# Performance work log

Hardware: AMD Instinct MI355X
Metric: run time of the kernel (lower is better)

Reference implementation:

```python
import jax, jax.numpy as jnp
import numpy as np

POI, EMB, UNITS, QDIM, B = 5000, 256, 512, 256, 64


def setup_inputs() -> dict:
    key = jax.random.key(0)
    ks = jax.random.split(key, 16)
    s = 0.05
    return {
        "x": jax.random.randint(ks[0], (B,), 0, POI),
        "query": jax.random.normal(ks[1], (B, QDIM), jnp.float32),
        "poi_embedding": jax.random.normal(ks[2], (POI, EMB), jnp.float32),
        "A_hat": jax.random.normal(ks[3], (B, B), jnp.float32),
        "dec_hidden": jax.random.normal(ks[4], (B, UNITS), jnp.float32),
        "cat_dec_hidden": jax.random.normal(ks[5], (1, B, UNITS), jnp.float32),
        # GRUCell params (keras order z, r, h; reset_after=True -> bias [2, 3*units])
        "gru_kernel": jax.random.normal(ks[6], (EMB + QDIM, 3 * UNITS), jnp.float32) * s,
        "gru_rec_kernel": jax.random.normal(ks[7], (UNITS, 3 * UNITS), jnp.float32) * s,
        "gru_bias": jax.random.normal(ks[8], (2, 3 * UNITS), jnp.float32) * s,
        # Bahdanau attention params
        "W1_w": jax.random.normal(ks[9], (EMB, UNITS), jnp.float32) * s,
        "W1_b": jnp.zeros((UNITS,), jnp.float32),
        "W2_w": jax.random.normal(ks[10], (UNITS, UNITS), jnp.float32) * s,
        "W2_b": jnp.zeros((UNITS,), jnp.float32),
        "V_w": jax.random.normal(ks[11], (UNITS, 1), jnp.float32) * s,
        "V_b": jnp.zeros((1,), jnp.float32),
        # output dense: concat(context EMB, output_ UNITS, cat_hidden UNITS) -> POI
        "fc_w": jax.random.normal(ks[12], (EMB + 2 * UNITS, POI), jnp.float32) * s,
        "fc_b": jnp.zeros((POI,), jnp.float32),
    }


def _gru_cell(x, h, kernel, rec_kernel, bias):
    # keras GRUCell, reset_after=True, gate order (z, r, h)
    xm = x @ kernel + bias[0]        # [B, 3U]
    hm = h @ rec_kernel + bias[1]    # [B, 3U]
    xz, xr, xh = jnp.split(xm, 3, axis=-1)
    hz, hr, hh = jnp.split(hm, 3, axis=-1)
    z = jax.nn.sigmoid(xz + hz)
    r = jax.nn.sigmoid(xr + hr)
    h_cand = jnp.tanh(xh + r * hh)
    h_new = z * h + (1.0 - z) * h_cand
    return h_new, h_new


def reference(x, query, poi_embedding, A_hat, dec_hidden, cat_dec_hidden,
              gru_kernel, gru_rec_kernel, gru_bias,
              W1_w, W1_b, W2_w, W2_b, V_w, V_b, fc_w, fc_b):
    emb = poi_embedding
    x1 = jnp.concatenate([emb[x], query], axis=1)          # [B, EMB+QDIM]
    output_, state = _gru_cell(x1, dec_hidden, gru_kernel, gru_rec_kernel, gru_bias)
    # Bahdanau attention: values are the full embedding table [POI, EMB]
    v_proj = emb @ W1_w + W1_b                              # [POI, U]
    q_proj = output_ @ W2_w + W2_b                          # [B, U]
    score = jnp.tanh(v_proj[None, :, :] + q_proj[:, None, :]) @ V_w + V_b  # [B, POI, 1]
    attn = jax.nn.softmax(score, axis=1)                    # [B, POI, 1]
    context = jnp.sum(attn * emb[None, :, :], axis=1)       # [B, EMB]
    out_cat = jnp.concatenate([context, output_, cat_dec_hidden[0]], axis=1)
    logits = out_cat @ fc_w + fc_b                          # [B, POI]
    return (logits, state, output_)
```

## Files before the change

kernel.cpp:

```cpp
#include <hip/hip_runtime.h>
#include <hip/hip_bf16.h>

typedef __bf16 bf16;
typedef __bf16 bf16x8 __attribute__((ext_vector_type(8)));
typedef float f32x4 __attribute__((ext_vector_type(4)));
typedef float f32x2 __attribute__((ext_vector_type(2)));

#define BB 64
#define EMB 256
#define UNITS 512
#define POI 5000
#define KCAT 1280
#define SCLD 5024
#define L2E 1.4426950408889634f

__device__ __forceinline__ float rcp_(float x){ return __builtin_amdgcn_rcpf(x); }
__device__ __forceinline__ float exp2_(float x){ return __builtin_amdgcn_exp2f(x); }

__device__ __forceinline__ bf16x8 cvt8(f32x4 a0, f32x4 a1){
  bf16x8 o;
#pragma unroll
  for(int j=0;j<4;j++){ o[j]=(bf16)a0[j]; o[4+j]=(bf16)a1[j]; }
  return o;
}

__device__ __forceinline__ f32x4 mm16r(const float* __restrict__ ap, const float* __restrict__ B,
                                       int ldb, int K, int nc, int lane){
  int q = lane >> 4;
  f32x4 acc = {0.f,0.f,0.f,0.f};
  ap += q*8;
  const float* bp = B + (size_t)(q*8)*ldb + nc;
#pragma unroll 2
  for(int k0 = 0; k0 < K; k0 += 32){
    bf16x8 a = cvt8(*(const f32x4*)ap, *(const f32x4*)(ap+4));
    bf16x8 b;
#pragma unroll
    for(int j=0;j<8;j++) b[j] = (bf16)bp[(size_t)j*ldb];
    acc = __builtin_amdgcn_mfma_f32_16x16x32_bf16(a, b, acc, 0, 0, 0);
    ap += 32; bp += (size_t)32*ldb;
  }
  return acc;
}
__device__ __forceinline__ f32x4 mm16f(const float* __restrict__ A, const float* __restrict__ B,
                                       int lda, int ldb, int K, int mr, int nc, int lane){
  return mm16r(A + (size_t)mr*lda, B, ldb, K, nc, lane);
}

__device__ __forceinline__ void t64(const float* __restrict__ src, int srcLd, int nRv,
    int r0, int c0, int cW, bf16* __restrict__ dstT, int dstLd,
    int lane, int w){
  int r = r0 + lane;
  bool rv = r < nRv;
  int cw4 = cW >> 2;
  int cb = c0 + w*cw4;
  for(int c8=0;c8<cw4;c8+=8){
    int c = cb + c8;
    f32x4 v0={0.f,0.f,0.f,0.f}, v1={0.f,0.f,0.f,0.f};
    if(rv){ v0 = *(const f32x4*)(src + (size_t)r*srcLd + c);
            v1 = *(const f32x4*)(src + (size_t)r*srcLd + c + 4); }
#pragma unroll
    for(int j=0;j<4;j++){
      dstT[(size_t)(c+j)*dstLd + r]   = (bf16)v0[j];
      dstT[(size_t)(c+4+j)*dstLd + r] = (bf16)v1[j];
    }
  }
}

__global__ __launch_bounds__(256) void k_prep0(
    const float* __restrict__ emb, const float* __restrict__ W1, const float* __restrict__ W2,
    const float* __restrict__ fcb, const float* __restrict__ catd,
    float* __restrict__ out, float* __restrict__ outc,
    bf16* __restrict__ embB, bf16* __restrict__ W1Tb, bf16* __restrict__ W2Tb,
    float* __restrict__ sumb, float* __restrict__ sc){
  int bx = blockIdx.x, t = threadIdx.x, lane = t & 63, w = t >> 6;
  if(bx < 80){
    int r0 = bx*64;
    for(int ch = t; ch < 2048; ch += 256){
      int r = r0 + (ch >> 5), cc = (ch & 31)*8;
      if(r < POI){
        f32x4 v0 = *(const f32x4*)(emb + (size_t)r*EMB + cc);
        f32x4 v1 = *(const f32x4*)(emb + (size_t)r*EMB + cc + 4);
        *(bf16x8*)(embB + (size_t)r*EMB + cc) = cvt8(v0, v1);
      }
    }
  } else if(bx < 88){
    int i = bx - 80;
    t64(W1, UNITS, EMB, (i>>1)*64, (i&1)*256, 256, W1Tb, EMB, lane, w);
  } else if(bx < 104){
    int i = bx - 88;
    t64(W2, UNITS, UNITS, (i>>1)*64, (i&1)*256, 256, W2Tb, UNITS, lane, w);
  } else if(bx < 168){
    int b = bx - 104;
    for(int n=t; n<POI; n+=256) out[(size_t)b*POI + n] = fcb[n];
  } else if(bx < 176){
    int base = (bx - 168)*8;
    for(int i=t; i<8*768; i+=256){
      int bb = base + i/768, c = i - (i/768)*768;
      if(c < 256) outc[(size_t)bb*KCAT + c] = 0.f;
      else        outc[(size_t)bb*KCAT + 512 + c] = catd[(size_t)bb*512 + (c-256)];
    }
  } else {
    if(t < BB) sumb[t] = 0.f;
    for(int i=t; i<BB*24; i+=256){
      int b = i/24, j = i - (i/24)*24;
      sc[(size_t)b*SCLD + POI + j] = 0.f;
    }
  }
}

__global__ __launch_bounds__(256) void k_gru(const int* __restrict__ x, const float* __restrict__ query,
    const bf16* __restrict__ embB, const float* __restrict__ h0,
    const float* __restrict__ gruK, const float* __restrict__ gruR,
    float* __restrict__ xmP, float* __restrict__ hmP){
  int lane = threadIdx.x & 63, w = threadIdx.x >> 6;
  int col = blockIdx.x*16 + (lane & 15);
  int y = blockIdx.y, z = blockIdx.z;
  int mr = w*16 + (lane & 15);
  int q = lane >> 4;
  const float* bp = (y ? gruR : gruK) + (size_t)(z*256 + q*8)*1536 + col;
  float* C = (y ? hmP : xmP) + (size_t)z*BB*1536;
  f32x4 acc = {0.f,0.f,0.f,0.f};
  if(y == 0 && z == 0){
    const bf16* ap = embB + (size_t)x[mr]*EMB + q*8;
#pragma unroll 2
    for(int k0=0;k0<256;k0+=32){
      bf16x8 a = *(const bf16x8*)ap;
      bf16x8 b;
#pragma unroll
      for(int j=0;j<8;j++) b[j] = (bf16)bp[(size_t)j*1536];
      acc = __builtin_amdgcn_mfma_f32_16x16x32_bf16(a, b, acc, 0,0,0);
      ap += 32; bp += (size_t)32*1536;
    }
  } else {
    const float* apf = y ? (h0 + (size_t)mr*512 + z*256 + q*8)
                         : (query + (size_t)mr*256 + q*8);
#pragma unroll 2
    for(int k0=0;k0<256;k0+=32){
      bf16x8 a = cvt8(*(const f32x4*)apf, *(const f32x4*)(apf+4));
      bf16x8 b;
#pragma unroll
      for(int j=0;j<8;j++) b[j] = (bf16)bp[(size_t)j*1536];
      acc = __builtin_amdgcn_mfma_f32_16x16x32_bf16(a, b, acc, 0,0,0);
      apf += 32; bp += (size_t)32*1536;
    }
  }
  int rb = w*16 + (lane >> 4)*4;
#pragma unroll
  for(int r=0;r<4;r++) C[(size_t)(rb+r)*1536 + col] = acc[r];
}

__global__ __launch_bounds__(256) void k_gates(const float* __restrict__ xmP, const float* __restrict__ hmP,
                        const float* __restrict__ bias, const float* __restrict__ h0,
                        float* __restrict__ hn, float* __restrict__ outc, float* __restrict__ dout){
  int b = blockIdx.x, u = blockIdx.y*256 + threadIdx.x;
  const float* x0 = xmP + b*1536; const float* x1s = xmP + (size_t)BB*1536 + b*1536;
  const float* h0s = hmP + b*1536; const float* h1s = hmP + (size_t)BB*1536 + b*1536;
  float xz = x0[u]      + x1s[u]      + bias[u];
  float xg = x0[512+u]  + x1s[512+u]  + bias[512+u];
  float xh = x0[1024+u] + x1s[1024+u] + bias[1024+u];
  float hz = h0s[u]      + h1s[u]      + bias[1536+u];
  float hg = h0s[512+u]  + h1s[512+u]  + bias[2048+u];
  float hh = h0s[1024+u] + h1s[1024+u] + bias[2560+u];
  float z = rcp_(1.f + exp2_(-L2E*(xz+hz)));
  float r = rcp_(1.f + exp2_(-L2E*(xg+hg)));
  float ca = xh + r*hh;
  ca = fminf(fmaxf(ca, -15.f), 15.f);
  float e = exp2_(2.f*L2E*ca);
  float hc = (e - 1.f)*rcp_(e + 1.f);
  float h = h0[(size_t)b*512+u];
  float v = z*h + (1.f - z)*hc;
  hn[(size_t)b*512+u] = v;
  outc[(size_t)b*KCAT + 256 + u] = v;
  dout[(size_t)POI*BB + (size_t)b*512 + u] = v;
  dout[(size_t)POI*BB + (size_t)BB*512 + (size_t)b*512 + u] = v;
}

__global__ __launch_bounds__(256) void k_qproj(const float* __restrict__ hn, const bf16* __restrict__ W2Tb,
                        const float* __restrict__ W2b, float* __restrict__ Eq){
  __shared__ float accs[16][17];
  int t = threadIdx.x, lane = t & 63, w = t >> 6;
  int c16 = blockIdx.x & 31, r16 = blockIdx.x >> 5;
  for(int i=t;i<16*17;i+=256) ((float*)accs)[i] = 0.f;
  __syncthreads();
  int q = lane >> 4;
  int mr  = r16*16 + (lane & 15);
  int col = c16*16 + (lane & 15);
  const float* ap = hn + (size_t)mr*UNITS + w*128 + q*8;
  const bf16*  bp = W2Tb + (size_t)col*UNITS + w*128 + q*8;
  f32x4 acc = {0.f,0.f,0.f,0.f};
#pragma unroll
  for(int k0=0;k0<128;k0+=32){
    bf16x8 a = cvt8(*(const f32x4*)ap, *(const f32x4*)(ap+4));
    bf16x8 b = *(const bf16x8*)bp;
    acc = __builtin_amdgcn_mfma_f32_16x16x32_bf16(a,b,acc,0,0,0);
    ap += 32; bp += 32;
  }
#pragma unroll
  for(int r=0;r<4;r++) atomicAdd(&accs[q*4+r][lane & 15], acc[r]);
  __syncthreads();
  int r = t >> 4, c = t & 15;
  int colg = c16*16 + c;
  float v = (accs[r][c] + W2b[colg])*(2.f*L2E);
  Eq[(size_t)(r16*16+r)*UNITS + colg] = exp2_(fminf(fmaxf(v,-40.f),40.f));
}

__global__ __launch_bounds__(512) void k_vscore(
    const bf16* __restrict__ embB, const bf16* __restrict__ W1Tb,
    const float* __restrict__ W1b, const float* __restrict__ Eq,
    const float* __restrict__ Vw, float* __restrict__ sc, float* __restrict__ sumb){
  __shared__ float evsT[512][20];
  __shared__ float vws[512];
  int t = threadIdx.x, lane = t & 63, w = t >> 6;
  int p0 = blockIdx.x*16;
  int q = lane >> 4;
  int mr = p0 + (lane & 15); if(mr > POI-1) mr = POI-1;
  bf16x8 afr[8];
  {
    const bf16* ap = embB + (size_t)mr*EMB + q*8;
#pragma unroll
    for(int k=0;k<8;k++){ afr[k] = *(const bf16x8*)ap; ap += 32; }
  }
#pragma unroll
  for(int i=0;i<4;i++){
    int colL = (w + 8*i)*16 + (lane & 15);
    const bf16* bp = W1Tb + (size_t)colL*EMB + q*8;
    f32x4 acc = {0.f,0.f,0.f,0.f};
#pragma unroll
    for(int k=0;k<8;k++){
      acc = __builtin_amdgcn_mfma_f32_16x16x32_bf16(afr[k], *(const bf16x8*)bp, acc, 0,0,0);
      bp += 32;
    }
    float bn = W1b[colL];
    f32x4 ev;
#pragma unroll
    for(int r=0;r<4;r++){
      float v = (acc[r] + bn)*(2.f*L2E);
      ev[r] = exp2_(fminf(fmaxf(v,-40.f),40.f));
    }
    *(f32x4*)&evsT[colL][q*4] = ev;
  }
  vws[t] = Vw[t];
  __syncthreads();
  int pg = t & 7, b = t >> 3;
  const float* qrow = Eq + (size_t)b*UNITS;
  f32x2 s = {0.f, 0.f};
#pragma unroll 4
  for(int u4=0; u4<128; ++u4){
    f32x4 q4 = *(const f32x4*)&qrow[u4*4];
    f32x4 wv = *(const f32x4*)&vws[u4*4];
#pragma unroll
    for(int j=0;j<4;j++){
      f32x2 ev = *(const f32x2*)&evsT[u4*4+j][2*pg];
      s[0] += wv[j]*rcp_(ev[0]*q4[j] + 1.f);
      s[1] += wv[j]*rcp_(ev[1]*q4[j] + 1.f);
    }
  }
  int pA = p0 + 2*pg;
  float e0 = (pA   < POI) ? exp2_(-2.f*L2E*s[0]) : 0.f;
  float e1 = (pA+1 < POI) ? exp2_(-2.f*L2E*s[1]) : 0.f;
  float* srow = sc + (size_t)b*SCLD + pA;
  if(pA+1 < POI){ f32x2 e2 = {e0, e1}; *(f32x2*)srow = e2; }
  else if(pA < POI) srow[0] = e0;
  float ps = e0 + e1;
  ps += __shfl_xor(ps, 1);
  ps += __shfl_xor(ps, 2);
  ps += __shfl_xor(ps, 4);
  if(pg == 0) atomicAdd(&sumb[b], ps);
}

__global__ __launch_bounds__(256) void k_ctx(const float* __restrict__ wb, const float* __restrict__ emb,
                                             const float* __restrict__ sumb, float* __restrict__ outc){
  int lane = threadIdx.x & 63, w = threadIdx.x >> 6;
  int n = blockIdx.x*16 + (lane & 15);
  int ky = blockIdx.y;
  int kbeg = ky*64;
  int mr = w*16 + (lane & 15);
  int q = lane >> 4;
  const float* ap = wb + (size_t)mr*SCLD + kbeg + q*8;
  f32x4 acc = {0.f,0.f,0.f,0.f};
  if(ky < 78){
    const float* bp = emb + (size_t)(kbeg + q*8)*EMB + n;
#pragma unroll 2
    for(int k0=0;k0<64;k0+=32){
      bf16x8 a = cvt8(*(const f32x4*)ap, *(const f32x4*)(ap+4));
      bf16x8 b;
#pragma unroll
      for(int j=0;j<8;j++) b[j] = (bf16)bp[(size_t)j*EMB];
      acc = __builtin_amdgcn_mfma_f32_16x16x32_bf16(a,b,acc,0,0,0);
      ap += 32; bp += (size_t)32*EMB;
    }
  } else {
    bf16x8 a = cvt8(*(const f32x4*)ap, *(const f32x4*)(ap+4));
    bf16x8 b;
#pragma unroll
    for(int j=0;j<8;j++){
      int k = kbeg + q*8 + j; int kc = k < POI ? k : POI-1;
      b[j] = (bf16)emb[(size_t)kc*EMB + n];
    }
    acc = __builtin_amdgcn_mfma_f32_16x16x32_bf16(a,b,acc,0,0,0);
  }
  int rb = w*16 + (lane >> 4)*4;
#pragma unroll
  for(int r=0;r<4;r++) atomicAdd(&outc[(size_t)(rb+r)*KCAT + n], acc[r]*rcp_(sumb[rb+r]));
}

__global__ __launch_bounds__(256) void k_logits(const float* __restrict__ A, const float* __restrict__ Bw,
                        float* __restrict__ out){
  int lane = threadIdx.x & 63, w = threadIdx.x >> 6;
  int n = blockIdx.x*16 + (lane & 15);
  int nc = n < POI ? n : POI-1;
  int ky = blockIdx.y, kbeg = ky*160;
  f32x4 acc = mm16f(A + kbeg, Bw + (size_t)kbeg*POI, KCAT, POI, 160,
                    w*16 + (lane & 15), nc, lane);
  int rb = w*16 + (lane >> 4)*4;
  if(n < POI){
#pragma unroll
    for(int r=0;r<4;r++) atomicAdd(&out[(size_t)(rb+r)*POI + n], acc[r]);
  }
}

extern "C" void kernel_launch(void* const* d_in, const int* in_sizes, int n_in,
                              void* d_out, int out_size, void* d_ws, size_t ws_size,
                              hipStream_t stream){
  const int*   x     = (const int*)d_in[0];
  const float* query = (const float*)d_in[1];
  const float* emb   = (const float*)d_in[2];
  const float* h0    = (const float*)d_in[4];
  const float* catd  = (const float*)d_in[5];
  const float* gruK  = (const float*)d_in[6];
  const float* gruR  = (const float*)d_in[7];
  const float* gruB  = (const float*)d_in[8];
  const float* W1    = (const float*)d_in[9];
  const float* W1b   = (const float*)d_in[10];
  const float* W2    = (const float*)d_in[11];
  const float* W2b   = (const float*)d_in[12];
  const float* Vw    = (const float*)d_in[13];
  const float* fcw   = (const float*)d_in[15];
  const float* fcb   = (const float*)d_in[16];
  float* out = (float*)d_out;

  char* ws = (char*)d_ws;
  size_t off = 0;
  auto alloc = [&](size_t bytes)->void*{ void* p = ws + off; off += (bytes + 255) & ~(size_t)255; return p; };
  float* outc   = (float*)alloc((size_t)BB*KCAT*4);
  float* xmP    = (float*)alloc((size_t)2*BB*1536*4);
  float* hmP    = (float*)alloc((size_t)2*BB*1536*4);
  float* hn     = (float*)alloc((size_t)BB*512*4);
  float* Eq     = (float*)alloc((size_t)BB*512*4);
  bf16*  embB   = (bf16*)alloc((size_t)POI*EMB*2);
  bf16*  W1Tb   = (bf16*)alloc((size_t)UNITS*EMB*2);
  bf16*  W2Tb   = (bf16*)alloc((size_t)UNITS*UNITS*2);
  float* sumb   = (float*)alloc((size_t)BB*4);
  float* sc     = (float*)alloc((size_t)BB*SCLD*4);

  k_prep0  <<<177, 256, 0, stream>>>(emb, W1, W2, fcb, catd, out, outc,
                                     embB, W1Tb, W2Tb, sumb, sc);
  k_gru    <<<dim3(96,2,2), 256, 0, stream>>>(x, query, embB, h0, gruK, gruR, xmP, hmP);
  k_gates  <<<dim3(BB,2), 256, 0, stream>>>(xmP, hmP, gruB, h0, hn, outc, out);
  k_qproj  <<<128, 256, 0, stream>>>(hn, W2Tb, W2b, Eq);
  k_vscore <<<313, 512, 0, stream>>>(embB, W1Tb, W1b, Eq, Vw, sc, sumb);
  k_ctx    <<<dim3(16,79), 256, 0, stream>>>(sc, emb, sumb, outc);
  k_logits <<<dim3(313,8), 256, 0, stream>>>(outc, fcw, out);
}
```

Measured before the change: 211.2 us.

## Split attention score over unit slices and add separate softmax-exp reduction kernel

```diff
diff --git a/kernel.cpp b/kernel.cpp
--- a/kernel.cpp
+++ b/kernel.cpp
@@ -4,7 +4,6 @@
 typedef __bf16 bf16;
 typedef __bf16 bf16x8 __attribute__((ext_vector_type(8)));
 typedef float f32x4 __attribute__((ext_vector_type(4)));
-typedef float f32x2 __attribute__((ext_vector_type(2)));
 
 #define BB 64
 #define EMB 256
@@ -204,33 +203,28 @@
   Eq[(size_t)(r16*16+r)*UNITS + colg] = exp2_(fminf(fmaxf(v,-40.f),40.f));
 }
 
-__global__ __launch_bounds__(512) void k_vscore(
+__global__ __launch_bounds__(256, 8) void k_vscore(
     const bf16* __restrict__ embB, const bf16* __restrict__ W1Tb,
     const float* __restrict__ W1b, const float* __restrict__ Eq,
-    const float* __restrict__ Vw, float* __restrict__ sc, float* __restrict__ sumb){
-  __shared__ float evsT[512][20];
-  __shared__ float vws[512];
+    const float* __restrict__ Vw, float* __restrict__ scS){
+  __shared__ float evsT[64][20];
+  __shared__ float vws[64];
   int t = threadIdx.x, lane = t & 63, w = t >> 6;
-  int p0 = blockIdx.x*16;
+  int p0 = blockIdx.x*16, uh = blockIdx.y*64;
   int q = lane >> 4;
   int mr = p0 + (lane & 15); if(mr > POI-1) mr = POI-1;
-  bf16x8 afr[8];
   {
+    int colL = w*16 + (lane & 15);
     const bf16* ap = embB + (size_t)mr*EMB + q*8;
-#pragma unroll
-    for(int k=0;k<8;k++){ afr[k] = *(const bf16x8*)ap; ap += 32; }
-  }
-#pragma unroll
-  for(int i=0;i<4;i++){
-    int colL = (w + 8*i)*16 + (lane & 15);
-    const bf16* bp = W1Tb + (size_t)colL*EMB + q*8;
+    const bf16* bp = W1Tb + (size_t)(uh+colL)*EMB + q*8;
     f32x4 acc = {0.f,0.f,0.f,0.f};
 #pragma unroll
-    for(int k=0;k<8;k++){
-      acc = __builtin_amdgcn_mfma_f32_16x16x32_bf16(afr[k], *(const bf16x8*)bp, acc, 0,0,0);
-      bp += 32;
-    }
-    float bn = W1b[colL];
+    for(int k0=0;k0<EMB;k0+=32){
+      bf16x8 a = *(const bf16x8*)ap, b = *(const bf16x8*)bp;
+      acc = __builtin_amdgcn_mfma_f32_16x16x32_bf16(a,b,acc,0,0,0);
+      ap += 32; bp += 32;
+    }
+    float bn = W1b[uh+colL];
     f32x4 ev;
 #pragma unroll
     for(int r=0;r<4;r++){
@@ -239,33 +233,49 @@
     }
     *(f32x4*)&evsT[colL][q*4] = ev;
   }
-  vws[t] = Vw[t];
+  if(t < 64) vws[t] = Vw[uh + t];
   __syncthreads();
-  int pg = t & 7, b = t >> 3;
-  const float* qrow = Eq + (size_t)b*UNITS;
-  f32x2 s = {0.f, 0.f};
+  int pg = t & 3, b = t >> 2;
+  const float* qrow = Eq + (size_t)b*UNITS + uh;
+  f32x4 s = {0.f,0.f,0.f,0.f};
 #pragma unroll 4
-  for(int u4=0; u4<128; ++u4){
+  for(int u4=0; u4<16; ++u4){
     f32x4 q4 = *(const f32x4*)&qrow[u4*4];
     f32x4 wv = *(const f32x4*)&vws[u4*4];
 #pragma unroll
     for(int j=0;j<4;j++){
-      f32x2 ev = *(const f32x2*)&evsT[u4*4+j][2*pg];
-      s[0] += wv[j]*rcp_(ev[0]*q4[j] + 1.f);
-      s[1] += wv[j]*rcp_(ev[1]*q4[j] + 1.f);
-    }
-  }
-  int pA = p0 + 2*pg;
-  float e0 = (pA   < POI) ? exp2_(-2.f*L2E*s[0]) : 0.f;
-  float e1 = (pA+1 < POI) ? exp2_(-2.f*L2E*s[1]) : 0.f;
-  float* srow = sc + (size_t)b*SCLD + pA;
-  if(pA+1 < POI){ f32x2 e2 = {e0, e1}; *(f32x2*)srow = e2; }
-  else if(pA < POI) srow[0] = e0;
-  float ps = e0 + e1;
-  ps += __shfl_xor(ps, 1);
-  ps += __shfl_xor(ps, 2);
-  ps += __shfl_xor(ps, 4);
-  if(pg == 0) atomicAdd(&sumb[b], ps);
+      f32x4 ev = *(const f32x4*)&evsT[u4*4+j][4*pg];
+#pragma unroll
+      for(int e=0;e<4;e++)
+        s[e] += wv[j]*rcp_(ev[e]*q4[j] + 1.f);
+    }
+  }
+  int pA = p0 + 4*pg;
+  float* srow = scS + (size_t)blockIdx.y*BB*SCLD + (size_t)b*SCLD + pA;
+  if(pA + 3 < POI) *(f32x4*)srow = s;
+  else {
+#pragma unroll
+    for(int e=0;e<4;e++) if(pA+e < POI) srow[e] = s[e];
+  }
+}
+
+__global__ __launch_bounds__(256) void k_smax(float* __restrict__ sc, float* __restrict__ sumb){
+  __shared__ float red[256];
+  int b = blockIdx.x, y = blockIdx.y, t = threadIdx.x;
+  float* sA = sc + (size_t)b*SCLD;
+  int pend = (y+1)*640; if(pend > POI) pend = POI;
+  float sm = 0.f;
+  for(int p = y*640 + t; p < pend; p += 256){
+    float acc = sA[p];
+#pragma unroll
+    for(int s2=1;s2<8;s2++) acc += sA[(size_t)s2*BB*SCLD + p];
+    float e = exp2_(-2.f*L2E*acc);
+    sA[p] = e;
+    sm += e;
+  }
+  red[t] = sm; __syncthreads();
+  for(int o=128;o>0;o>>=1){ if(t<o) red[t]+=red[t+o]; __syncthreads(); }
+  if(t==0) atomicAdd(sumb + b, red[0]);
 }
 
 __global__ __launch_bounds__(256) void k_ctx(const float* __restrict__ wb, const float* __restrict__ emb,
@@ -309,8 +319,8 @@
   int lane = threadIdx.x & 63, w = threadIdx.x >> 6;
   int n = blockIdx.x*16 + (lane & 15);
   int nc = n < POI ? n : POI-1;
-  int ky = blockIdx.y, kbeg = ky*160;
-  f32x4 acc = mm16f(A + kbeg, Bw + (size_t)kbeg*POI, KCAT, POI, 160,
+  int ky = blockIdx.y, kbeg = ky*320;
+  f32x4 acc = mm16f(A + kbeg, Bw + (size_t)kbeg*POI, KCAT, POI, 320,
                     w*16 + (lane & 15), nc, lane);
   int rb = w*16 + (lane >> 4)*4;
   if(n < POI){
@@ -351,14 +361,15 @@
   bf16*  W1Tb   = (bf16*)alloc((size_t)UNITS*EMB*2);
   bf16*  W2Tb   = (bf16*)alloc((size_t)UNITS*UNITS*2);
   float* sumb   = (float*)alloc((size_t)BB*4);
-  float* sc     = (float*)alloc((size_t)BB*SCLD*4);
+  float* sc     = (float*)alloc((size_t)8*BB*SCLD*4);
 
   k_prep0  <<<177, 256, 0, stream>>>(emb, W1, W2, fcb, catd, out, outc,
                                      embB, W1Tb, W2Tb, sumb, sc);
   k_gru    <<<dim3(96,2,2), 256, 0, stream>>>(x, query, embB, h0, gruK, gruR, xmP, hmP);
   k_gates  <<<dim3(BB,2), 256, 0, stream>>>(xmP, hmP, gruB, h0, hn, outc, out);
   k_qproj  <<<128, 256, 0, stream>>>(hn, W2Tb, W2b, Eq);
-  k_vscore <<<313, 512, 0, stream>>>(embB, W1Tb, W1b, Eq, Vw, sc, sumb);
+  k_vscore <<<dim3(313,8), 256, 0, stream>>>(embB, W1Tb, W1b, Eq, Vw, sc);
+  k_smax   <<<dim3(BB,8), 256, 0, stream>>>(sc, sumb);
   k_ctx    <<<dim3(16,79), 256, 0, stream>>>(sc, emb, sumb, outc);
-  k_logits <<<dim3(313,8), 256, 0, stream>>>(outc, fcw, out);
-}
+  k_logits <<<dim3(313,4), 256, 0, stream>>>(outc, fcw, out);
+}
```

New measurement: 191.2 us, median of 2. 1.1x faster.
